# Kernel tuning notes

Measured on AMD Instinct MI355X. Metric: run time of the kernel, lower is better.

The kernel has to match this reference:

```python
import jax, jax.numpy as jnp
import numpy as np


def _pairwise_sqdist(a, b):
    # a: [B,N,3], b: [B,M,3] -> [B,N,M] squared L2 distances
    a2 = jnp.sum(a * a, axis=-1)            # [B,N]
    b2 = jnp.sum(b * b, axis=-1)            # [B,M]
    ab = jnp.einsum('bnd,bmd->bnm', a, b)   # [B,N,M]
    d = a2[:, :, None] + b2[:, None, :] - 2.0 * ab
    return jnp.maximum(d, 0.0)


def setup_inputs() -> dict:
    key = jax.random.key(0)
    k1, k2 = jax.random.split(key)
    B, N, M = 4, 8192, 8192
    p1 = jax.random.normal(k1, (B, N, 3), dtype=jnp.float32)
    p2 = jax.random.normal(k2, (B, M, 3), dtype=jnp.float32)
    return {"p1": p1, "p2": p2}


def reference(p1, p2):
    # chamfer_3DDist: squared L2 NN distances both directions, then mean of each
    d = _pairwise_sqdist(p1, p2)   # [B,N,M]
    d1 = jnp.min(d, axis=2)        # [B,N] nearest p2 for each p1 point
    d2 = jnp.min(d, axis=1)        # [B,M] nearest p1 for each p2 point
    return jnp.mean(d1) + jnp.mean(d2)
```

## Files before the change

kernel.cpp:

```cpp
#include <hip/hip_runtime.h>
#include <float.h>


#define BLK   256
#define QPT   2
#define QPB   (BLK * QPT)
#define BATCH 4
#define NPTS  8192
#define NCH   8
#define CHUNK (NPTS / NCH)
#define QTILES (NPTS / QPB)
#define GRID  (2 * BATCH * QTILES * NCH)
#define TOTQ  (2 * BATCH * NPTS)

__global__ __launch_bounds__(BLK) void init_kernel(unsigned* mins, int n) {
    int i = blockIdx.x * BLK + threadIdx.x;
    if (i < n) mins[i] = 0x7F7FFFFFu;
}

__global__ __launch_bounds__(BLK, 4) void cd_chunk_kernel(
    const float* __restrict__ p1, const float* __restrict__ p2,
    unsigned* __restrict__ mins)
{
    __shared__ float4 pts[CHUNK];
    int bid    = blockIdx.x;
    int mchunk = bid & (NCH - 1);
    int qt     = (bid >> 3) & (QTILES - 1);
    int batch  = (bid >> 7) & (BATCH - 1);
    int dir    = bid >> 9;

    const float* qbase = (dir == 0 ? p1 : p2) + (size_t)batch * NPTS * 3;
    const float* dbase = (dir == 0 ? p2 : p1) + (size_t)batch * NPTS * 3;

    int tid = threadIdx.x;

    {
        int t4 = tid * 4;
        const float* s = dbase + (size_t)(mchunk * CHUNK + t4) * 3;
        float4 f0 = *(const float4*)(s);
        float4 f1 = *(const float4*)(s + 4);
        float4 f2 = *(const float4*)(s + 8);
        float x0 = f0.x, y0 = f0.y, z0 = f0.z;
        float x1 = f0.w, y1 = f1.x, z1 = f1.y;
        float x2 = f1.z, y2 = f1.w, z2 = f2.x;
        float x3 = f2.y, y3 = f2.z, z3 = f2.w;
        pts[t4 + 0] = make_float4(x0, y0, z0, -0.5f * (x0*x0 + y0*y0 + z0*z0));
        pts[t4 + 1] = make_float4(x1, y1, z1, -0.5f * (x1*x1 + y1*y1 + z1*z1));
        pts[t4 + 2] = make_float4(x2, y2, z2, -0.5f * (x2*x2 + y2*y2 + z2*z2));
        pts[t4 + 3] = make_float4(x3, y3, z3, -0.5f * (x3*x3 + y3*y3 + z3*z3));
    }

    int q0 = qt * QPB + tid;
    int q1 = q0 + BLK;
    float ax = qbase[q0 * 3 + 0], ay = qbase[q0 * 3 + 1], az = qbase[q0 * 3 + 2];
    float bx = qbase[q1 * 3 + 0], by = qbase[q1 * 3 + 1], bz = qbase[q1 * 3 + 2];
    float an = ax * ax + ay * ay + az * az;
    float bn = bx * bx + by * by + bz * bz;
    __syncthreads();

    float sa0 = -FLT_MAX, sa1 = -FLT_MAX;
    float sb0 = -FLT_MAX, sb1 = -FLT_MAX;

    #pragma unroll 2
    for (int j = 0; j < CHUNK; j += 4) {
        float4 u0 = pts[j + 0];
        float4 u1 = pts[j + 1];
        float4 u2 = pts[j + 2];
        float4 u3 = pts[j + 3];

        float a0 = fmaf(az, u0.z, fmaf(ay, u0.y, fmaf(ax, u0.x, u0.w)));
        float a1 = fmaf(az, u1.z, fmaf(ay, u1.y, fmaf(ax, u1.x, u1.w)));
        float a2 = fmaf(az, u2.z, fmaf(ay, u2.y, fmaf(ax, u2.x, u2.w)));
        float a3 = fmaf(az, u3.z, fmaf(ay, u3.y, fmaf(ax, u3.x, u3.w)));
        sa0 = fmaxf(sa0, fmaxf(a0, a1));
        sa1 = fmaxf(sa1, fmaxf(a2, a3));

        float b0 = fmaf(bz, u0.z, fmaf(by, u0.y, fmaf(bx, u0.x, u0.w)));
        float b1 = fmaf(bz, u1.z, fmaf(by, u1.y, fmaf(bx, u1.x, u1.w)));
        float b2 = fmaf(bz, u2.z, fmaf(by, u2.y, fmaf(bx, u2.x, u2.w)));
        float b3 = fmaf(bz, u3.z, fmaf(by, u3.y, fmaf(bx, u3.x, u3.w)));
        sb0 = fmaxf(sb0, fmaxf(b0, b1));
        sb1 = fmaxf(sb1, fmaxf(b2, b3));
    }

    float da = fmaxf(an - 2.f * fmaxf(sa0, sa1), 0.f);
    float db = fmaxf(bn - 2.f * fmaxf(sb0, sb1), 0.f);

    unsigned qid = (unsigned)(dir * (BATCH * NPTS) + batch * NPTS + q0);
    atomicMin(&mins[qid], __float_as_uint(da));
    atomicMin(&mins[qid + BLK], __float_as_uint(db));
}

__global__ __launch_bounds__(BLK) void sum_kernel(
    const unsigned* __restrict__ mins, float* __restrict__ out, int n, float scale)
{
    int i = blockIdx.x * BLK + threadIdx.x;
    int stride = gridDim.x * BLK;
    float v = 0.f;
    for (int idx = i; idx < n; idx += stride) v += __uint_as_float(mins[idx]);
    for (int off = 32; off > 0; off >>= 1) v += __shfl_down(v, off, 64);
    __shared__ float wsum[BLK / 64];
    int lane = threadIdx.x & 63, wid = threadIdx.x >> 6;
    if (lane == 0) wsum[wid] = v;
    __syncthreads();
    if (threadIdx.x == 0) {
        float t = 0.f;
        for (int w = 0; w < BLK / 64; ++w) t += wsum[w];
        atomicAdd(out, t * scale);
    }
}

__global__ void zero_out_kernel(float* out) { out[0] = 0.f; }

__global__ __launch_bounds__(BLK) void cd_full_kernel(
    const float* __restrict__ p1, const float* __restrict__ p2,
    float* __restrict__ out)
{
    __shared__ float4 pts[2048];
    int bid   = blockIdx.x;
    int qt    = bid & 15;
    int batch = (bid >> 4) & 3;
    int dir   = bid >> 6;

    const float* qbase = (dir == 0 ? p1 : p2) + (size_t)batch * NPTS * 3;
    const float* dbase = (dir == 0 ? p2 : p1) + (size_t)batch * NPTS * 3;

    int tid = threadIdx.x;
    int q0 = qt * 512 + tid;
    int q1 = q0 + BLK;
    float ax = qbase[q0 * 3 + 0], ay = qbase[q0 * 3 + 1], az = qbase[q0 * 3 + 2];
    float bx = qbase[q1 * 3 + 0], by = qbase[q1 * 3 + 1], bz = qbase[q1 * 3 + 2];
    float an = ax * ax + ay * ay + az * az;
    float bn = bx * bx + by * by + bz * bz;

    float sa = -FLT_MAX, sb = -FLT_MAX;
    for (int c = 0; c < 4; ++c) {
        __syncthreads();
        int mstart = c * 2048;
        for (int j = tid; j < 2048; j += BLK) {
            const float* s = dbase + (size_t)(mstart + j) * 3;
            float x = s[0], y = s[1], z = s[2];
            pts[j] = make_float4(x, y, z, -0.5f * (x * x + y * y + z * z));
        }
        __syncthreads();
        #pragma unroll 4
        for (int j = 0; j < 2048; j += 2) {
            float4 u = pts[j];
            float4 v = pts[j + 1];
            float s;
            s = fmaf(ax, u.x, u.w); s = fmaf(ay, u.y, s); s = fmaf(az, u.z, s); sa = fmaxf(sa, s);
            s = fmaf(bx, u.x, u.w); s = fmaf(by, u.y, s); s = fmaf(bz, u.z, s); sb = fmaxf(sb, s);
            s = fmaf(ax, v.x, v.w); s = fmaf(ay, v.y, s); s = fmaf(az, v.z, s); sa = fmaxf(sa, s);
            s = fmaf(bx, v.x, v.w); s = fmaf(by, v.y, s); s = fmaf(bz, v.z, s); sb = fmaxf(sb, s);
        }
    }
    float da = fmaxf(an - 2.f * sa, 0.f);
    float db = fmaxf(bn - 2.f * sb, 0.f);
    float v = da + db;
    for (int off = 32; off > 0; off >>= 1) v += __shfl_down(v, off, 64);
    __shared__ float wsum[BLK / 64];
    int lane = threadIdx.x & 63, wid = threadIdx.x >> 6;
    if (lane == 0) wsum[wid] = v;
    __syncthreads();
    if (threadIdx.x == 0) {
        float t = 0.f;
        for (int w = 0; w < BLK / 64; ++w) t += wsum[w];
        atomicAdd(out, t * (1.f / (float)(BATCH * NPTS)));
    }
}

extern "C" void kernel_launch(void* const* d_in, const int* in_sizes, int n_in,
                              void* d_out, int out_size, void* d_ws, size_t ws_size,
                              hipStream_t stream) {
    const float* p1 = (const float*)d_in[0];
    const float* p2 = (const float*)d_in[1];
    float* out = (float*)d_out;

    if (ws_size >= (size_t)TOTQ * sizeof(unsigned)) {
        unsigned* mins = (unsigned*)d_ws;
        init_kernel<<<TOTQ / BLK, BLK, 0, stream>>>(mins, TOTQ);
        zero_out_kernel<<<1, 1, 0, stream>>>(out);
        cd_chunk_kernel<<<GRID, BLK, 0, stream>>>(p1, p2, mins);
        sum_kernel<<<64, BLK, 0, stream>>>(mins, out, TOTQ, 1.f / (float)(BATCH * NPTS));
    } else {
        zero_out_kernel<<<1, 1, 0, stream>>>(out);
        cd_full_kernel<<<128, BLK, 0, stream>>>(p1, p2, out);
    }
}
```

Baseline: 107.0 us.

## Register-tile four queries per thread, prefetch LDS points, fuse output zeroing

Each thread now handles four query points instead of two, so every candidate point read from LDS feeds twice as many distance evaluations. To keep the grid at the same block count, the candidate set is split into sixteen smaller chunks, and only part of the block loads the shared tile. The inner loop now loads the next four LDS points into registers while it computes on the current four. Zeroing the output moves into the init kernel, which removes one launch. The costs are higher register pressure (the occupancy hint in the launch bounds was dropped) and twice as many atomicMin operations per query across chunks.

```diff
diff --git a/kernel.cpp b/kernel.cpp
--- a/kernel.cpp
+++ b/kernel.cpp
@@ -3,29 +3,30 @@
 
 
 #define BLK   256
-#define QPT   2
+#define QPT   4
 #define QPB   (BLK * QPT)
 #define BATCH 4
 #define NPTS  8192
-#define NCH   8
+#define NCH   16
 #define CHUNK (NPTS / NCH)
 #define QTILES (NPTS / QPB)
 #define GRID  (2 * BATCH * QTILES * NCH)
 #define TOTQ  (2 * BATCH * NPTS)
 
-__global__ __launch_bounds__(BLK) void init_kernel(unsigned* mins, int n) {
+__global__ __launch_bounds__(BLK) void init_kernel(unsigned* mins, float* out, int n) {
     int i = blockIdx.x * BLK + threadIdx.x;
     if (i < n) mins[i] = 0x7F7FFFFFu;
+    if (i == 0) out[0] = 0.f;
 }
 
-__global__ __launch_bounds__(BLK, 4) void cd_chunk_kernel(
+__global__ __launch_bounds__(BLK) void cd_chunk_kernel(
     const float* __restrict__ p1, const float* __restrict__ p2,
     unsigned* __restrict__ mins)
 {
     __shared__ float4 pts[CHUNK];
     int bid    = blockIdx.x;
     int mchunk = bid & (NCH - 1);
-    int qt     = (bid >> 3) & (QTILES - 1);
+    int qt     = (bid >> 4) & (QTILES - 1);
     int batch  = (bid >> 7) & (BATCH - 1);
     int dir    = bid >> 9;
 
@@ -34,7 +35,7 @@
 
     int tid = threadIdx.x;
 
-    {
+    if (tid < CHUNK / 4) {
         int t4 = tid * 4;
         const float* s = dbase + (size_t)(mchunk * CHUNK + t4) * 3;
         float4 f0 = *(const float4*)(s);
@@ -50,45 +51,54 @@
         pts[t4 + 3] = make_float4(x3, y3, z3, -0.5f * (x3*x3 + y3*y3 + z3*z3));
     }
 
-    int q0 = qt * QPB + tid;
-    int q1 = q0 + BLK;
-    float ax = qbase[q0 * 3 + 0], ay = qbase[q0 * 3 + 1], az = qbase[q0 * 3 + 2];
-    float bx = qbase[q1 * 3 + 0], by = qbase[q1 * 3 + 1], bz = qbase[q1 * 3 + 2];
-    float an = ax * ax + ay * ay + az * az;
-    float bn = bx * bx + by * by + bz * bz;
+    float qx[QPT], qy[QPT], qz[QPT], qn[QPT];
+    #pragma unroll
+    for (int k = 0; k < QPT; ++k) {
+        int q = qt * QPB + k * BLK + tid;
+        const float* s = qbase + (size_t)q * 3;
+        qx[k] = s[0]; qy[k] = s[1]; qz[k] = s[2];
+        qn[k] = qx[k] * qx[k] + qy[k] * qy[k] + qz[k] * qz[k];
+    }
     __syncthreads();
 
-    float sa0 = -FLT_MAX, sa1 = -FLT_MAX;
-    float sb0 = -FLT_MAX, sb1 = -FLT_MAX;
+    float s0[QPT], s1[QPT];
+    #pragma unroll
+    for (int k = 0; k < QPT; ++k) { s0[k] = -FLT_MAX; s1[k] = -FLT_MAX; }
 
+    float4 c0 = pts[0], c1 = pts[1], c2 = pts[2], c3 = pts[3];
     #pragma unroll 2
-    for (int j = 0; j < CHUNK; j += 4) {
-        float4 u0 = pts[j + 0];
-        float4 u1 = pts[j + 1];
-        float4 u2 = pts[j + 2];
-        float4 u3 = pts[j + 3];
-
-        float a0 = fmaf(az, u0.z, fmaf(ay, u0.y, fmaf(ax, u0.x, u0.w)));
-        float a1 = fmaf(az, u1.z, fmaf(ay, u1.y, fmaf(ax, u1.x, u1.w)));
-        float a2 = fmaf(az, u2.z, fmaf(ay, u2.y, fmaf(ax, u2.x, u2.w)));
-        float a3 = fmaf(az, u3.z, fmaf(ay, u3.y, fmaf(ax, u3.x, u3.w)));
-        sa0 = fmaxf(sa0, fmaxf(a0, a1));
-        sa1 = fmaxf(sa1, fmaxf(a2, a3));
-
-        float b0 = fmaf(bz, u0.z, fmaf(by, u0.y, fmaf(bx, u0.x, u0.w)));
-        float b1 = fmaf(bz, u1.z, fmaf(by, u1.y, fmaf(bx, u1.x, u1.w)));
-        float b2 = fmaf(bz, u2.z, fmaf(by, u2.y, fmaf(bx, u2.x, u2.w)));
-        float b3 = fmaf(bz, u3.z, fmaf(by, u3.y, fmaf(bx, u3.x, u3.w)));
-        sb0 = fmaxf(sb0, fmaxf(b0, b1));
-        sb1 = fmaxf(sb1, fmaxf(b2, b3));
+    for (int j = 0; j < CHUNK - 4; j += 4) {
+        float4 n0 = pts[j + 4];
+        float4 n1 = pts[j + 5];
+        float4 n2 = pts[j + 6];
+        float4 n3 = pts[j + 7];
+        #pragma unroll
+        for (int k = 0; k < QPT; ++k) {
+            float d0 = fmaf(qz[k], c0.z, fmaf(qy[k], c0.y, fmaf(qx[k], c0.x, c0.w)));
+            float d1 = fmaf(qz[k], c1.z, fmaf(qy[k], c1.y, fmaf(qx[k], c1.x, c1.w)));
+            float d2 = fmaf(qz[k], c2.z, fmaf(qy[k], c2.y, fmaf(qx[k], c2.x, c2.w)));
+            float d3 = fmaf(qz[k], c3.z, fmaf(qy[k], c3.y, fmaf(qx[k], c3.x, c3.w)));
+            s0[k] = fmaxf(s0[k], fmaxf(d0, d1));
+            s1[k] = fmaxf(s1[k], fmaxf(d2, d3));
+        }
+        c0 = n0; c1 = n1; c2 = n2; c3 = n3;
+    }
+    #pragma unroll
+    for (int k = 0; k < QPT; ++k) {
+        float d0 = fmaf(qz[k], c0.z, fmaf(qy[k], c0.y, fmaf(qx[k], c0.x, c0.w)));
+        float d1 = fmaf(qz[k], c1.z, fmaf(qy[k], c1.y, fmaf(qx[k], c1.x, c1.w)));
+        float d2 = fmaf(qz[k], c2.z, fmaf(qy[k], c2.y, fmaf(qx[k], c2.x, c2.w)));
+        float d3 = fmaf(qz[k], c3.z, fmaf(qy[k], c3.y, fmaf(qx[k], c3.x, c3.w)));
+        s0[k] = fmaxf(s0[k], fmaxf(d0, d1));
+        s1[k] = fmaxf(s1[k], fmaxf(d2, d3));
     }
 
-    float da = fmaxf(an - 2.f * fmaxf(sa0, sa1), 0.f);
-    float db = fmaxf(bn - 2.f * fmaxf(sb0, sb1), 0.f);
-
-    unsigned qid = (unsigned)(dir * (BATCH * NPTS) + batch * NPTS + q0);
-    atomicMin(&mins[qid], __float_as_uint(da));
-    atomicMin(&mins[qid + BLK], __float_as_uint(db));
+    unsigned qid = (unsigned)(dir * (BATCH * NPTS) + batch * NPTS + qt * QPB + tid);
+    #pragma unroll
+    for (int k = 0; k < QPT; ++k) {
+        float d = fmaxf(qn[k] - 2.f * fmaxf(s0[k], s1[k]), 0.f);
+        atomicMin(&mins[qid + k * BLK], __float_as_uint(d));
+    }
 }
 
 __global__ __launch_bounds__(BLK) void sum_kernel(
@@ -178,8 +188,7 @@
 
     if (ws_size >= (size_t)TOTQ * sizeof(unsigned)) {
         unsigned* mins = (unsigned*)d_ws;
-        init_kernel<<<TOTQ / BLK, BLK, 0, stream>>>(mins, TOTQ);
-        zero_out_kernel<<<1, 1, 0, stream>>>(out);
+        init_kernel<<<TOTQ / BLK, BLK, 0, stream>>>(mins, out, TOTQ);
         cd_chunk_kernel<<<GRID, BLK, 0, stream>>>(p1, p2, mins);
         sum_kernel<<<64, BLK, 0, stream>>>(mins, out, TOTQ, 1.f / (float)(BATCH * NPTS));
     } else {
```

New measurement: 98.52 us. 7.9% less time.
